# Optimization experiments

Measured on AMD Instinct MI355X. Metric: run time of the kernel, lower is better.

Reference implementation:

```python
import jax, jax.numpy as jnp
import numpy as np

SQRT_2PI = (2.0 * 3.14159) ** 0.5  # matches torch.jit.script gaussian constant


def setup_inputs() -> dict:
    key = jax.random.key(0)
    ks = jax.random.split(key, 7)
    B, N, R, K, H, HEADS = 4, 256, 4, 128, 512, 32
    rpe = jax.random.uniform(ks[0], (B, N, N, R), dtype=jnp.float32) * 5.0
    means = jax.random.uniform(ks[1], (R, K), dtype=jnp.float32, minval=0.0, maxval=3.0)
    stds = jax.random.uniform(ks[2], (R, K), dtype=jnp.float32, minval=0.0, maxval=3.0)
    W1 = jax.random.normal(ks[3], (H, R * K), dtype=jnp.float32) * (1.0 / (R * K) ** 0.5)
    b1 = jax.random.normal(ks[4], (H,), dtype=jnp.float32) * 0.01
    W2 = jax.random.normal(ks[5], (HEADS, H), dtype=jnp.float32) * (1.0 / H ** 0.5)
    b2 = jax.random.normal(ks[6], (HEADS,), dtype=jnp.float32) * 0.01
    return {"rpe": rpe, "means": means, "stds": stds, "W1": W1, "b1": b1, "W2": W2, "b2": b2}


def reference(rpe, means, stds, W1, b1, W2, b2):
    # GaussianLayer: (B,N,N,R) -> (B,N,N,R*K)
    std = jnp.abs(stds) + 0.01                      # (R,K)
    x = rpe[..., None]                              # (B,N,N,R,1)
    g = jnp.exp(-0.5 * ((x - means) / std) ** 2) / (SQRT_2PI * std)  # (B,N,N,R,K)
    B, N = rpe.shape[0], rpe.shape[1]
    g = g.reshape(B, N, N, -1)                      # (B,N,N,R*K)
    # NonLinear MLP: Linear -> gelu(exact) -> Linear
    h = jax.nn.gelu(jnp.einsum('bmnf,hf->bmnh', g, W1) + b1, approximate=False)
    out = jnp.einsum('bmnh,oh->bmno', h, W2) + b2   # (B,N,N,heads)
    # permute BATCH_HEAD_NODE_NODE = (0,3,1,2)
    return jnp.transpose(out, (0, 3, 1, 2))
```

## Files before the change

kernel.cpp:

```cpp
#include <hip/hip_runtime.h>
#include <hip/hip_bf16.h>

typedef __attribute__((ext_vector_type(8))) short bfrag8;
typedef __attribute__((ext_vector_type(4))) float f32x4;
typedef __attribute__((ext_vector_type(4))) unsigned int u32x4;

#define IS2_SCALE 0.84932180028801907f
#define W1_SCALE  0.46971724f

#if __has_builtin(__builtin_amdgcn_exp2f)
#define GEXP(x) __builtin_amdgcn_exp2f(x)
#else
__device__ __forceinline__ float gexp_asm(float x) {
  float r; asm("v_exp_f32 %0, %1" : "=v"(r) : "v"(x)); return r;
}
#define GEXP(x) gexp_asm(x)
#endif

__device__ __forceinline__ unsigned short f2bf(float x) {
  union { float f; unsigned u; } v; v.f = x;
  unsigned r = v.u + 0x7fffu + ((v.u >> 16) & 1u);
  return (unsigned short)(r >> 16);
}
__device__ __forceinline__ unsigned cvtpk(float lo, float hi) {
  unsigned r;
  asm("v_cvt_pk_bf16_f32 %0, %1, %2" : "=v"(r) : "v"(lo), "v"(hi));
  return r;
}
__device__ __forceinline__ float rcpa(float x) {
  float r; asm("v_rcp_f32 %0, %1" : "=v"(r) : "v"(x)); return r;
}
__device__ __forceinline__ float gelu_fast(float x) {
  float x2 = x * x;
  float w = __builtin_fmaf(x2, -0.1029488f, -2.3022078f);
  float e = GEXP(x * w);
  return x * rcpa(e + 1.0f);
}

__global__ void prep_kernel(const float* __restrict__ means, const float* __restrict__ stds,
                            const float* __restrict__ W1, const float* __restrict__ W2,
                            unsigned short* __restrict__ W1bf, unsigned short* __restrict__ W2bf,
                            float* __restrict__ prm ) {
  int t = blockIdx.x * blockDim.x + threadIdx.x;
  int stride = gridDim.x * blockDim.x;
  for (int i = t; i < 512 * 512; i += stride) W1bf[i] = f2bf(W1[i] * W1_SCALE);
  for (int i = t; i < 32 * 512; i += stride) W2bf[i] = f2bf(W2[i]);
  for (int i = t; i < 512; i += stride) {
    float s = fabsf(stds[i]) + 0.01f;
    float is2 = (1.0f / s) * IS2_SCALE;
    prm[2 * i] = -means[i] * is2;
    prm[2 * i + 1] = is2;
  }
}

__global__ __launch_bounds__(1024, 4) void fused_kernel(
    const float* __restrict__ rpe, const unsigned short* __restrict__ W1bf,
    const unsigned short* __restrict__ W2bf, const float* __restrict__ prm,
    const float* __restrict__ b1, const float* __restrict__ b2,
    float* __restrict__ out) {
  __shared__ __attribute__((aligned(16))) char lds[131072 + 4096 + 2048 + 2048];
  float* prm_s = (float*)(lds + 131072);
  float* rpe_s = (float*)(lds + 131072 + 4096);
  float* b1_s  = (float*)(lds + 131072 + 4096 + 2048);

  const int tid = threadIdx.x;
  const int rb = blockIdx.x * 128;

  if (tid < 512) rpe_s[tid] = rpe[rb * 4 + tid];
  prm_s[tid] = prm[tid];
  if (tid < 512) b1_s[tid] = b1[tid];

  int goff[2];
#pragma unroll
  for (int i = 0; i < 2; ++i) {
    int c = i * 1024 + tid;
    int j = ((c >> 6) << 4) + (c & 15);
    goff[i] = j * 512 + ((c >> 4) & 3) * 8;
  }
  const char* Wc = (const char*)W1bf;

#define STAGE(buf, kb)                                                          \
  {                                                                             \
    _Pragma("unroll") for (int i_ = 0; i_ < 2; ++i_) {                          \
      const void* gp = (const void*)(Wc + (size_t)goff[i_] * 2 + (kb) * 64);    \
      void* lp = (void*)(lds + (buf) * 32768 + i_ * 16384 + tid * 16);          \
      __builtin_amdgcn_global_load_lds(                                         \
          (const __attribute__((address_space(1))) void*)gp,                    \
          (__attribute__((address_space(3))) void*)lp, 16, 0, 0);               \
    }                                                                           \
  }

  STAGE(0, 0);
  __syncthreads();

  const int w = tid >> 6, l = tid & 63;
  const int lr = l & 15, lg = l >> 4;
  const int mw = w >> 2, nw = w & 3;
  const int r0 = mw * 32 + lr;

  const f32x4 xa = *(const f32x4*)&rpe_s[r0 * 4];
  const f32x4 xb = *(const f32x4*)&rpe_s[(r0 + 16) * 4];

  f32x4 zv = {0.f, 0.f, 0.f, 0.f};
  f32x4 acc[2][8];
#pragma unroll
  for (int mf = 0; mf < 2; ++mf)
#pragma unroll
    for (int nf = 0; nf < 8; ++nf) acc[mf][nf] = zv;

  const f32x4* prm4 = (const f32x4*)prm_s;
  int cur = 0;

#pragma unroll
  for (int kb = 0; kb < 16; ++kb) {
    if (kb < 15) STAGE(cur ^ 1, kb + 1);

    const int k0 = kb * 32 + lg * 8;
    const float x0 = xa[kb >> 2];
    const float x1 = xb[kb >> 2];
    unsigned pk0[4], pk1[4];
#pragma unroll
    for (int q = 0; q < 4; ++q) {
      f32x4 P = prm4[(k0 >> 1) + q];
      float u00 = __builtin_fmaf(x0, P[1], P[0]);
      float u01 = __builtin_fmaf(x0, P[3], P[2]);
      float u10 = __builtin_fmaf(x1, P[1], P[0]);
      float u11 = __builtin_fmaf(x1, P[3], P[2]);
      pk0[q] = cvtpk(P[1] * GEXP(-(u00 * u00)), P[3] * GEXP(-(u01 * u01)));
      pk1[q] = cvtpk(P[1] * GEXP(-(u10 * u10)), P[3] * GEXP(-(u11 * u11)));
    }
    u32x4 av0 = {pk0[0], pk0[1], pk0[2], pk0[3]};
    u32x4 av1 = {pk1[0], pk1[1], pk1[2], pk1[3]};
    bfrag8 a0 = __builtin_bit_cast(bfrag8, av0);
    bfrag8 a1 = __builtin_bit_cast(bfrag8, av1);

    if (kb < 15) {
      asm volatile("s_waitcnt vmcnt(2)" ::: "memory");
    } else {
      asm volatile("s_waitcnt vmcnt(0)" ::: "memory");
    }
    __builtin_amdgcn_s_barrier();
    __builtin_amdgcn_sched_barrier(0);

    const char* Bbase = lds + cur * 32768 + nw * 8192 + lg * 256 + lr * 16;
    __builtin_amdgcn_s_setprio(1);
#pragma unroll
    for (int nf = 0; nf < 8; ++nf) {
      bfrag8 b = *(const bfrag8*)(Bbase + nf * 1024);
      acc[0][nf] = __builtin_amdgcn_mfma_f32_16x16x32_bf16(a0, b, acc[0][nf], 0, 0, 0);
      acc[1][nf] = __builtin_amdgcn_mfma_f32_16x16x32_bf16(a1, b, acc[1][nf], 0, 0, 0);
    }
    __builtin_amdgcn_s_setprio(0);

    __builtin_amdgcn_s_barrier();
    cur ^= 1;
  }

  unsigned short* hbuf = (unsigned short*)lds;
#pragma unroll
  for (int mf = 0; mf < 2; ++mf) {
#pragma unroll
    for (int nf = 0; nf < 8; nf += 2) {
      int col0 = nw * 128 + nf * 16 + lr;
      int col1 = col0 + 16;
      float bb0 = b1_s[col0], bb1 = b1_s[col1];
#pragma unroll
      for (int bi = 0; bi < 4; ++bi) {
        float g0 = gelu_fast(acc[mf][nf][bi] + bb0);
        float g1 = gelu_fast(acc[mf][nf + 1][bi] + bb1);
        unsigned pr = cvtpk(g0, g1);
        int hrow = mw * 32 + mf * 16 + lg * 4 + bi;
        int base = hrow * 1024, sw = (hrow & 7) << 4;
        *(unsigned short*)((char*)hbuf + base + ((col0 * 2) ^ sw)) = (unsigned short)pr;
        *(unsigned short*)((char*)hbuf + base + ((col1 * 2) ^ sw)) = (unsigned short)(pr >> 16);
      }
    }
  }
  __syncthreads();

  const int rt = w >> 1, ct = w & 1;
  f32x4 acc2 = zv;
  const int row2 = rt * 16 + lr;
  for (int kb = 0; kb < 16; ++kb) {
    int cb = (kb * 64 + lg * 16) ^ ((row2 & 7) << 4);
    bfrag8 a = *(const bfrag8*)((char*)hbuf + row2 * 1024 + cb);
    bfrag8 b = *(const bfrag8*)(W2bf + (size_t)(ct * 16 + lr) * 512 + kb * 32 + lg * 8);
    acc2 = __builtin_amdgcn_mfma_f32_16x16x32_bf16(a, b, acc2, 0, 0, 0);
  }
  float b2v = b2[ct * 16 + lr];
  __syncthreads();

  float* ob = (float*)lds;
#pragma unroll
  for (int bi = 0; bi < 4; ++bi)
    ob[(rt * 16 + lg * 4 + bi) * 33 + (ct * 16 + lr)] = acc2[bi] + b2v;
  __syncthreads();

  const int bI = rb >> 16, mI = (rb >> 8) & 255, n0 = rb & 255;
  float* obase = out + ((size_t)(bI * 32) * 256 + mI) * 256 + n0;
#pragma unroll
  for (int p = 0; p < 4; ++p) {
    int e = tid + p * 1024;
    int o = e >> 7, i = e & 127;
    obase[(size_t)o * 65536 + i] = ob[i * 33 + o];
  }
#undef STAGE
}

extern "C" void kernel_launch(void* const* d_in, const int* in_sizes, int n_in,
                              void* d_out, int out_size, void* d_ws, size_t ws_size,
                              hipStream_t stream) {
  const float* rpe   = (const float*)d_in[0];
  const float* means = (const float*)d_in[1];
  const float* stds  = (const float*)d_in[2];
  const float* W1    = (const float*)d_in[3];
  const float* b1    = (const float*)d_in[4];
  const float* W2    = (const float*)d_in[5];
  const float* b2    = (const float*)d_in[6];
  float* out = (float*)d_out;

  char* ws = (char*)d_ws;
  unsigned short* W1bf = (unsigned short*)ws;
  unsigned short* W2bf = (unsigned short*)(ws + 524288);
  float* prm = (float*)(ws + 557056);

  prep_kernel<<<256, 256, 0, stream>>>(means, stds, W1, W2, W1bf, W2bf, prm);
  fused_kernel<<<2048, 1024, 0, stream>>>(rpe, W1bf, W2bf, prm, b1, b2, out);
}
```

Baseline: 276.0 us.

## Compute Gaussian A-fragments once per row group and share via LDS

Previously each of the four N-waves sharing the same rows recomputed the identical Gaussian basis fragments every k-step. Now only nw==0 waves compute them, one step ahead, and write them into a double-buffered 16KB LDS slot that the other waves read. This removes 3/4 of the exp/fma work but puts that work on a quarter of the waves, adds LDS traffic and a waitcnt, and raises LDS use per block, which may affect occupancy and balance. Note that gsl is indexed by lg*2048 + r0*16, and r0 only reaches 127 (2032 bytes), so the layout fits within the slot.

```diff
diff --git a/kernel.cpp b/kernel.cpp
--- a/kernel.cpp
+++ b/kernel.cpp
@@ -35,6 +35,27 @@
   float w = __builtin_fmaf(x2, -0.1029488f, -2.3022078f);
   float e = GEXP(x * w);
   return x * rcpa(e + 1.0f);
+}
+
+__device__ __forceinline__ void gauss_frags(const f32x4* prm4, const f32x4 xa, const f32x4 xb,
+                                            int kb, int lg, bfrag8* A0, bfrag8* A1) {
+  const int k0 = kb * 32 + lg * 8;
+  const float x0 = xa[kb >> 2], x1 = xb[kb >> 2];
+  unsigned pk0[4], pk1[4];
+#pragma unroll
+  for (int q = 0; q < 4; ++q) {
+    f32x4 P = prm4[(k0 >> 1) + q];
+    float u00 = __builtin_fmaf(x0, P[1], P[0]);
+    float u01 = __builtin_fmaf(x0, P[3], P[2]);
+    float u10 = __builtin_fmaf(x1, P[1], P[0]);
+    float u11 = __builtin_fmaf(x1, P[3], P[2]);
+    pk0[q] = cvtpk(P[1] * GEXP(-(u00 * u00)), P[3] * GEXP(-(u01 * u01)));
+    pk1[q] = cvtpk(P[1] * GEXP(-(u10 * u10)), P[3] * GEXP(-(u11 * u11)));
+  }
+  u32x4 av0 = {pk0[0], pk0[1], pk0[2], pk0[3]};
+  u32x4 av1 = {pk1[0], pk1[1], pk1[2], pk1[3]};
+  *A0 = __builtin_bit_cast(bfrag8, av0);
+  *A1 = __builtin_bit_cast(bfrag8, av1);
 }
 
 __global__ void prep_kernel(const float* __restrict__ means, const float* __restrict__ stds,
@@ -58,10 +79,11 @@
     const unsigned short* __restrict__ W2bf, const float* __restrict__ prm,
     const float* __restrict__ b1, const float* __restrict__ b2,
     float* __restrict__ out) {
-  __shared__ __attribute__((aligned(16))) char lds[131072 + 4096 + 2048 + 2048];
+  __shared__ __attribute__((aligned(16))) char lds[131072 + 4096 + 2048 + 2048 + 16384];
   float* prm_s = (float*)(lds + 131072);
   float* rpe_s = (float*)(lds + 131072 + 4096);
   float* b1_s  = (float*)(lds + 131072 + 4096 + 2048);
+  char*  gsl   = lds + 131072 + 4096 + 2048 + 2048;
 
   const int tid = threadIdx.x;
   const int rb = blockIdx.x * 128;
@@ -100,6 +122,18 @@
 
   const f32x4 xa = *(const f32x4*)&rpe_s[r0 * 4];
   const f32x4 xb = *(const f32x4*)&rpe_s[(r0 + 16) * 4];
+  const f32x4* prm4 = (const f32x4*)prm_s;
+
+  char* gw = gsl + lg * 2048 + r0 * 16;
+  const char* gr = gsl + lg * 2048 + r0 * 16;
+
+  bfrag8 acur0, acur1;
+  if (nw == 0) {
+    gauss_frags(prm4, xa, xb, 0, lg, &acur0, &acur1);
+    *(bfrag8*)(gw) = acur0;
+    *(bfrag8*)(gw + 256) = acur1;
+  }
+  __syncthreads();
 
   f32x4 zv = {0.f, 0.f, 0.f, 0.f};
   f32x4 acc[2][8];
@@ -108,31 +142,27 @@
 #pragma unroll
     for (int nf = 0; nf < 8; ++nf) acc[mf][nf] = zv;
 
-  const f32x4* prm4 = (const f32x4*)prm_s;
   int cur = 0;
 
 #pragma unroll
   for (int kb = 0; kb < 16; ++kb) {
     if (kb < 15) STAGE(cur ^ 1, kb + 1);
 
-    const int k0 = kb * 32 + lg * 8;
-    const float x0 = xa[kb >> 2];
-    const float x1 = xb[kb >> 2];
-    unsigned pk0[4], pk1[4];
-#pragma unroll
-    for (int q = 0; q < 4; ++q) {
-      f32x4 P = prm4[(k0 >> 1) + q];
-      float u00 = __builtin_fmaf(x0, P[1], P[0]);
-      float u01 = __builtin_fmaf(x0, P[3], P[2]);
-      float u10 = __builtin_fmaf(x1, P[1], P[0]);
-      float u11 = __builtin_fmaf(x1, P[3], P[2]);
-      pk0[q] = cvtpk(P[1] * GEXP(-(u00 * u00)), P[3] * GEXP(-(u01 * u01)));
-      pk1[q] = cvtpk(P[1] * GEXP(-(u10 * u10)), P[3] * GEXP(-(u11 * u11)));
-    }
-    u32x4 av0 = {pk0[0], pk0[1], pk0[2], pk0[3]};
-    u32x4 av1 = {pk1[0], pk1[1], pk1[2], pk1[3]};
-    bfrag8 a0 = __builtin_bit_cast(bfrag8, av0);
-    bfrag8 a1 = __builtin_bit_cast(bfrag8, av1);
+    const int slot = (kb & 1) * 8192;
+    bfrag8 a0, a1, an0, an1;
+    if (nw == 0) {
+      a0 = acur0; a1 = acur1;
+      if (kb < 15) {
+        gauss_frags(prm4, xa, xb, kb + 1, lg, &an0, &an1);
+        char* gwn = gw + (((kb + 1) & 1) * 8192);
+        *(bfrag8*)(gwn) = an0;
+        *(bfrag8*)(gwn + 256) = an1;
+        asm volatile("s_waitcnt lgkmcnt(0)" ::: "memory");
+      }
+    } else {
+      a0 = *(const bfrag8*)(gr + slot);
+      a1 = *(const bfrag8*)(gr + slot + 256);
+    }
 
     if (kb < 15) {
       asm volatile("s_waitcnt vmcnt(2)" ::: "memory");
@@ -153,6 +183,7 @@
     __builtin_amdgcn_s_setprio(0);
 
     __builtin_amdgcn_s_barrier();
+    if (nw == 0 && kb < 15) { acur0 = an0; acur1 = an1; }
     cur ^= 1;
   }
 
```

After: 281.7 us. 1.02x slower.

## Split hidden dimension across blocks with atomic accumulation of second GEMM

Applied to the files above, without the earlier changes.

Each block now processes 512 rows for one quarter of the hidden units, loading its entire W1 slice into LDS once instead of double-buffering K tiles. The second linear layer is computed per hidden-quarter and partial results are added into the output with fp32 atomics, after a new kernel initializes the output with b2. This removes per-tile barriers and the cross-wave hidden buffer, but quadruples Gaussian feature computation, adds an extra full output write pass and atomic traffic, and makes summation order nondeterministic.

```diff
diff --git a/kernel.cpp b/kernel.cpp
--- a/kernel.cpp
+++ b/kernel.cpp
@@ -35,6 +35,27 @@
   float w = __builtin_fmaf(x2, -0.1029488f, -2.3022078f);
   float e = GEXP(x * w);
   return x * rcpa(e + 1.0f);
+}
+
+__device__ __forceinline__ void gauss_frags(const f32x4* prm4, const f32x4 xa, const f32x4 xb,
+                                            int kb, int lg, bfrag8* A0, bfrag8* A1) {
+  const int k0 = kb * 32 + lg * 8;
+  const float x0 = xa[kb >> 2], x1 = xb[kb >> 2];
+  unsigned pk0[4], pk1[4];
+#pragma unroll
+  for (int q = 0; q < 4; ++q) {
+    f32x4 P = prm4[(k0 >> 1) + q];
+    float u00 = __builtin_fmaf(x0, P[1], P[0]);
+    float u01 = __builtin_fmaf(x0, P[3], P[2]);
+    float u10 = __builtin_fmaf(x1, P[1], P[0]);
+    float u11 = __builtin_fmaf(x1, P[3], P[2]);
+    pk0[q] = cvtpk(P[1] * GEXP(-(u00 * u00)), P[3] * GEXP(-(u01 * u01)));
+    pk1[q] = cvtpk(P[1] * GEXP(-(u10 * u10)), P[3] * GEXP(-(u11 * u11)));
+  }
+  u32x4 av0 = {pk0[0], pk0[1], pk0[2], pk0[3]};
+  u32x4 av1 = {pk1[0], pk1[1], pk1[2], pk1[3]};
+  *A0 = __builtin_bit_cast(bfrag8, av0);
+  *A1 = __builtin_bit_cast(bfrag8, av1);
 }
 
 __global__ void prep_kernel(const float* __restrict__ means, const float* __restrict__ stds,
@@ -53,158 +74,122 @@
   }
 }
 
+__global__ void init_out(const float* __restrict__ b2, float* __restrict__ out) {
+  int i = blockIdx.x * blockDim.x + threadIdx.x;
+  float v = b2[(i >> 14) & 31];
+  f32x4 vv = {v, v, v, v};
+  *reinterpret_cast<f32x4*>(out + (size_t)i * 4) = vv;
+}
+
 __global__ __launch_bounds__(1024, 4) void fused_kernel(
     const float* __restrict__ rpe, const unsigned short* __restrict__ W1bf,
     const unsigned short* __restrict__ W2bf, const float* __restrict__ prm,
-    const float* __restrict__ b1, const float* __restrict__ b2,
-    float* __restrict__ out) {
-  __shared__ __attribute__((aligned(16))) char lds[131072 + 4096 + 2048 + 2048];
+    const float* __restrict__ b1, float* __restrict__ out) {
+  __shared__ __attribute__((aligned(16))) char lds[131072 + 4096];
   float* prm_s = (float*)(lds + 131072);
-  float* rpe_s = (float*)(lds + 131072 + 4096);
-  float* b1_s  = (float*)(lds + 131072 + 4096 + 2048);
 
   const int tid = threadIdx.x;
-  const int rb = blockIdx.x * 128;
-
-  if (tid < 512) rpe_s[tid] = rpe[rb * 4 + tid];
+  const int bid = blockIdx.x;
+  const int c = bid & 3;
+  const int rb = (bid >> 2) * 512;
+
   prm_s[tid] = prm[tid];
-  if (tid < 512) b1_s[tid] = b1[tid];
-
-  int goff[2];
-#pragma unroll
-  for (int i = 0; i < 2; ++i) {
-    int c = i * 1024 + tid;
-    int j = ((c >> 6) << 4) + (c & 15);
-    goff[i] = j * 512 + ((c >> 4) & 3) * 8;
-  }
+
   const char* Wc = (const char*)W1bf;
-
-#define STAGE(buf, kb)                                                          \
-  {                                                                             \
-    _Pragma("unroll") for (int i_ = 0; i_ < 2; ++i_) {                          \
-      const void* gp = (const void*)(Wc + (size_t)goff[i_] * 2 + (kb) * 64);    \
-      void* lp = (void*)(lds + (buf) * 32768 + i_ * 16384 + tid * 16);          \
-      __builtin_amdgcn_global_load_lds(                                         \
-          (const __attribute__((address_space(1))) void*)gp,                    \
-          (__attribute__((address_space(3))) void*)lp, 16, 0, 0);               \
-    }                                                                           \
-  }
-
-  STAGE(0, 0);
+#pragma unroll
+  for (int i = 0; i < 8; ++i) {
+    int c16 = i * 1024 + tid;
+    int ks = c16 >> 9;
+    int J  = (c16 >> 6) & 7;
+    int lgs = (c16 >> 4) & 3;
+    int jr = c16 & 15;
+    const void* gp = Wc + ((size_t)(c * 128 + J * 16 + jr) * 512 + ks * 32 + lgs * 8) * 2;
+    void* lp = lds + c16 * 16;
+    __builtin_amdgcn_global_load_lds(
+        (const __attribute__((address_space(1))) void*)gp,
+        (__attribute__((address_space(3))) void*)lp, 16, 0, 0);
+  }
   __syncthreads();
 
   const int w = tid >> 6, l = tid & 63;
   const int lr = l & 15, lg = l >> 4;
-  const int mw = w >> 2, nw = w & 3;
-  const int r0 = mw * 32 + lr;
-
-  const f32x4 xa = *(const f32x4*)&rpe_s[r0 * 4];
-  const f32x4 xb = *(const f32x4*)&rpe_s[(r0 + 16) * 4];
+  const int r0w = rb + w * 32;
+
+  const f32x4 xa = *(const f32x4*)(rpe + (size_t)(r0w + lr) * 4);
+  const f32x4 xb = *(const f32x4*)(rpe + (size_t)(r0w + 16 + lr) * 4);
+  const f32x4* prm4 = (const f32x4*)prm_s;
 
   f32x4 zv = {0.f, 0.f, 0.f, 0.f};
   f32x4 acc[2][8];
 #pragma unroll
   for (int mf = 0; mf < 2; ++mf)
 #pragma unroll
-    for (int nf = 0; nf < 8; ++nf) acc[mf][nf] = zv;
-
-  const f32x4* prm4 = (const f32x4*)prm_s;
-  int cur = 0;
-
-#pragma unroll
-  for (int kb = 0; kb < 16; ++kb) {
-    if (kb < 15) STAGE(cur ^ 1, kb + 1);
-
-    const int k0 = kb * 32 + lg * 8;
-    const float x0 = xa[kb >> 2];
-    const float x1 = xb[kb >> 2];
-    unsigned pk0[4], pk1[4];
-#pragma unroll
-    for (int q = 0; q < 4; ++q) {
-      f32x4 P = prm4[(k0 >> 1) + q];
-      float u00 = __builtin_fmaf(x0, P[1], P[0]);
-      float u01 = __builtin_fmaf(x0, P[3], P[2]);
-      float u10 = __builtin_fmaf(x1, P[1], P[0]);
-      float u11 = __builtin_fmaf(x1, P[3], P[2]);
-      pk0[q] = cvtpk(P[1] * GEXP(-(u00 * u00)), P[3] * GEXP(-(u01 * u01)));
-      pk1[q] = cvtpk(P[1] * GEXP(-(u10 * u10)), P[3] * GEXP(-(u11 * u11)));
+    for (int J = 0; J < 8; ++J) acc[mf][J] = zv;
+
+#pragma unroll
+  for (int ks = 0; ks < 16; ++ks) {
+    bfrag8 a0, a1;
+    gauss_frags(prm4, xa, xb, ks, lg, &a0, &a1);
+    const char* Bb = lds + ks * 8192 + lg * 256 + lr * 16;
+#pragma unroll
+    for (int J = 0; J < 8; ++J) {
+      bfrag8 b = *(const bfrag8*)(Bb + J * 1024);
+      acc[0][J] = __builtin_amdgcn_mfma_f32_16x16x32_bf16(a0, b, acc[0][J], 0, 0, 0);
+      acc[1][J] = __builtin_amdgcn_mfma_f32_16x16x32_bf16(a1, b, acc[1][J], 0, 0, 0);
     }
-    u32x4 av0 = {pk0[0], pk0[1], pk0[2], pk0[3]};
-    u32x4 av1 = {pk1[0], pk1[1], pk1[2], pk1[3]};
-    bfrag8 a0 = __builtin_bit_cast(bfrag8, av0);
-    bfrag8 a1 = __builtin_bit_cast(bfrag8, av1);
-
-    if (kb < 15) {
-      asm volatile("s_waitcnt vmcnt(2)" ::: "memory");
-    } else {
-      asm volatile("s_waitcnt vmcnt(0)" ::: "memory");
-    }
-    __builtin_amdgcn_s_barrier();
-    __builtin_amdgcn_sched_barrier(0);
-
-    const char* Bbase = lds + cur * 32768 + nw * 8192 + lg * 256 + lr * 16;
-    __builtin_amdgcn_s_setprio(1);
-#pragma unroll
-    for (int nf = 0; nf < 8; ++nf) {
-      bfrag8 b = *(const bfrag8*)(Bbase + nf * 1024);
-      acc[0][nf] = __builtin_amdgcn_mfma_f32_16x16x32_bf16(a0, b, acc[0][nf], 0, 0, 0);
-      acc[1][nf] = __builtin_amdgcn_mfma_f32_16x16x32_bf16(a1, b, acc[1][nf], 0, 0, 0);
-    }
-    __builtin_amdgcn_s_setprio(0);
-
-    __builtin_amdgcn_s_barrier();
-    cur ^= 1;
-  }
-
-  unsigned short* hbuf = (unsigned short*)lds;
+  }
+  __syncthreads();
+
+  char* scr = lds + w * 8192;
 #pragma unroll
   for (int mf = 0; mf < 2; ++mf) {
 #pragma unroll
-    for (int nf = 0; nf < 8; nf += 2) {
-      int col0 = nw * 128 + nf * 16 + lr;
-      int col1 = col0 + 16;
-      float bb0 = b1_s[col0], bb1 = b1_s[col1];
-#pragma unroll
-      for (int bi = 0; bi < 4; ++bi) {
-        float g0 = gelu_fast(acc[mf][nf][bi] + bb0);
-        float g1 = gelu_fast(acc[mf][nf + 1][bi] + bb1);
-        unsigned pr = cvtpk(g0, g1);
-        int hrow = mw * 32 + mf * 16 + lg * 4 + bi;
-        int base = hrow * 1024, sw = (hrow & 7) << 4;
-        *(unsigned short*)((char*)hbuf + base + ((col0 * 2) ^ sw)) = (unsigned short)pr;
-        *(unsigned short*)((char*)hbuf + base + ((col1 * 2) ^ sw)) = (unsigned short)(pr >> 16);
+    for (int J = 0; J < 8; ++J) {
+      float bb = b1[c * 128 + J * 16 + lr];
+#pragma unroll
+      for (int q = 0; q < 4; ++q) {
+        float g = gelu_fast(acc[mf][J][q] + bb);
+        int r = mf * 16 + lg * 4 + q;
+        int byte = (r * 256 + (J * 16 + lr) * 2) ^ ((r & 7) << 4);
+        *(unsigned short*)(scr + byte) = f2bf(g);
       }
     }
   }
-  __syncthreads();
-
-  const int rt = w >> 1, ct = w & 1;
-  f32x4 acc2 = zv;
-  const int row2 = rt * 16 + lr;
-  for (int kb = 0; kb < 16; ++kb) {
-    int cb = (kb * 64 + lg * 16) ^ ((row2 & 7) << 4);
-    bfrag8 a = *(const bfrag8*)((char*)hbuf + row2 * 1024 + cb);
-    bfrag8 b = *(const bfrag8*)(W2bf + (size_t)(ct * 16 + lr) * 512 + kb * 32 + lg * 8);
-    acc2 = __builtin_amdgcn_mfma_f32_16x16x32_bf16(a, b, acc2, 0, 0, 0);
-  }
-  float b2v = b2[ct * 16 + lr];
-  __syncthreads();
-
-  float* ob = (float*)lds;
-#pragma unroll
-  for (int bi = 0; bi < 4; ++bi)
-    ob[(rt * 16 + lg * 4 + bi) * 33 + (ct * 16 + lr)] = acc2[bi] + b2v;
-  __syncthreads();
-
-  const int bI = rb >> 16, mI = (rb >> 8) & 255, n0 = rb & 255;
-  float* obase = out + ((size_t)(bI * 32) * 256 + mI) * 256 + n0;
-#pragma unroll
-  for (int p = 0; p < 4; ++p) {
-    int e = tid + p * 1024;
-    int o = e >> 7, i = e & 127;
-    obase[(size_t)o * 65536 + i] = ob[i * 33 + o];
-  }
-#undef STAGE
+
+  bfrag8 w2f[2][4];
+#pragma unroll
+  for (int og = 0; og < 2; ++og)
+#pragma unroll
+    for (int kk = 0; kk < 4; ++kk)
+      w2f[og][kk] = *(const bfrag8*)(W2bf + (size_t)(og * 16 + lr) * 512 + c * 128 + kk * 32 + lg * 8);
+
+  asm volatile("s_waitcnt lgkmcnt(0)" ::: "memory");
+  f32x4 acc2[2][2];
+  acc2[0][0] = zv; acc2[0][1] = zv; acc2[1][0] = zv; acc2[1][1] = zv;
+#pragma unroll
+  for (int rf = 0; rf < 2; ++rf) {
+#pragma unroll
+    for (int kk = 0; kk < 4; ++kk) {
+      int r = rf * 16 + lr;
+      int byte = (r * 256 + kk * 64 + lg * 16) ^ ((r & 7) << 4);
+      bfrag8 a = *(const bfrag8*)(scr + byte);
+      acc2[rf][0] = __builtin_amdgcn_mfma_f32_16x16x32_bf16(a, w2f[0][kk], acc2[rf][0], 0, 0, 0);
+      acc2[rf][1] = __builtin_amdgcn_mfma_f32_16x16x32_bf16(a, w2f[1][kk], acc2[rf][1], 0, 0, 0);
+    }
+  }
+
+  const int bI = rb >> 16;
+  float* ob = out + (size_t)bI * 2097152 + (rb & 65535) + w * 32;
+#pragma unroll
+  for (int rf = 0; rf < 2; ++rf)
+#pragma unroll
+    for (int og = 0; og < 2; ++og)
+#pragma unroll
+      for (int q = 0; q < 4; ++q) {
+        int o = og * 16 + lr;
+        int r = rf * 16 + lg * 4 + q;
+        atomicAdd(ob + (size_t)o * 65536 + r, acc2[rf][og][q]);
+      }
 }
 
 extern "C" void kernel_launch(void* const* d_in, const int* in_sizes, int n_in,
@@ -225,5 +210,6 @@
   float* prm = (float*)(ws + 557056);
 
   prep_kernel<<<256, 256, 0, stream>>>(means, stds, W1, W2, W1bf, W2bf, prm);
-  fused_kernel<<<2048, 1024, 0, stream>>>(rpe, W1bf, W2bf, prm, b1, b2, out);
-}
+  init_out<<<8192, 256, 0, stream>>>(b2, out);
+  fused_kernel<<<2048, 1024, 0, stream>>>(rpe, W1bf, W2bf, prm, b1, out);
+}
```

New measurement: 505.3 us. +83.0%, slower.

## Triple-buffer W1 LDS tiles and software-pipeline B fragments and Gaussian features

Applied to the files above, without the earlier changes.

The first GEMM's K-loop moves from double to triple buffering of W1 tiles in LDS, prefetching two stages ahead with a single barrier per iteration instead of two. B fragments are split into two register halves so the next stage's first half is read from LDS while the second half's MFMAs run. The Gaussian A-fragments for the next K-block are computed after the current MFMAs to overlap VALU exp work with matrix work. The cost is higher register pressure from the extra fragment buffers and a full vmcnt(0) wait each iteration.

```diff
diff --git a/kernel.cpp b/kernel.cpp
--- a/kernel.cpp
+++ b/kernel.cpp
@@ -35,6 +35,27 @@
   float w = __builtin_fmaf(x2, -0.1029488f, -2.3022078f);
   float e = GEXP(x * w);
   return x * rcpa(e + 1.0f);
+}
+
+__device__ __forceinline__ void gauss_frags(const f32x4* prm4, const f32x4 xa, const f32x4 xb,
+                                            int kb, int lg, bfrag8* A0, bfrag8* A1) {
+  const int k0 = kb * 32 + lg * 8;
+  const float x0 = xa[kb >> 2], x1 = xb[kb >> 2];
+  unsigned pk0[4], pk1[4];
+#pragma unroll
+  for (int q = 0; q < 4; ++q) {
+    f32x4 P = prm4[(k0 >> 1) + q];
+    float u00 = __builtin_fmaf(x0, P[1], P[0]);
+    float u01 = __builtin_fmaf(x0, P[3], P[2]);
+    float u10 = __builtin_fmaf(x1, P[1], P[0]);
+    float u11 = __builtin_fmaf(x1, P[3], P[2]);
+    pk0[q] = cvtpk(P[1] * GEXP(-(u00 * u00)), P[3] * GEXP(-(u01 * u01)));
+    pk1[q] = cvtpk(P[1] * GEXP(-(u10 * u10)), P[3] * GEXP(-(u11 * u11)));
+  }
+  u32x4 av0 = {pk0[0], pk0[1], pk0[2], pk0[3]};
+  u32x4 av1 = {pk1[0], pk1[1], pk1[2], pk1[3]};
+  *A0 = __builtin_bit_cast(bfrag8, av0);
+  *A1 = __builtin_bit_cast(bfrag8, av1);
 }
 
 __global__ void prep_kernel(const float* __restrict__ means, const float* __restrict__ stds,
@@ -91,6 +112,7 @@
   }
 
   STAGE(0, 0);
+  STAGE(1, 1);
   __syncthreads();
 
   const int w = tid >> 6, l = tid & 63;
@@ -100,6 +122,7 @@
 
   const f32x4 xa = *(const f32x4*)&rpe_s[r0 * 4];
   const f32x4 xb = *(const f32x4*)&rpe_s[(r0 + 16) * 4];
+  const f32x4* prm4 = (const f32x4*)prm_s;
 
   f32x4 zv = {0.f, 0.f, 0.f, 0.f};
   f32x4 acc[2][8];
@@ -108,53 +131,50 @@
 #pragma unroll
     for (int nf = 0; nf < 8; ++nf) acc[mf][nf] = zv;
 
-  const f32x4* prm4 = (const f32x4*)prm_s;
-  int cur = 0;
+  bfrag8 fA[4], fB[4];
+  {
+    const char* Bb = lds + nw * 8192 + lg * 256 + lr * 16;
+#pragma unroll
+    for (int nf = 0; nf < 4; ++nf) fA[nf] = *(const bfrag8*)(Bb + nf * 1024);
+  }
+  bfrag8 a0, a1;
+  gauss_frags(prm4, xa, xb, 0, lg, &a0, &a1);
 
 #pragma unroll
   for (int kb = 0; kb < 16; ++kb) {
-    if (kb < 15) STAGE(cur ^ 1, kb + 1);
-
-    const int k0 = kb * 32 + lg * 8;
-    const float x0 = xa[kb >> 2];
-    const float x1 = xb[kb >> 2];
-    unsigned pk0[4], pk1[4];
-#pragma unroll
-    for (int q = 0; q < 4; ++q) {
-      f32x4 P = prm4[(k0 >> 1) + q];
-      float u00 = __builtin_fmaf(x0, P[1], P[0]);
-      float u01 = __builtin_fmaf(x0, P[3], P[2]);
-      float u10 = __builtin_fmaf(x1, P[1], P[0]);
-      float u11 = __builtin_fmaf(x1, P[3], P[2]);
-      pk0[q] = cvtpk(P[1] * GEXP(-(u00 * u00)), P[3] * GEXP(-(u01 * u01)));
-      pk1[q] = cvtpk(P[1] * GEXP(-(u10 * u10)), P[3] * GEXP(-(u11 * u11)));
-    }
-    u32x4 av0 = {pk0[0], pk0[1], pk0[2], pk0[3]};
-    u32x4 av1 = {pk1[0], pk1[1], pk1[2], pk1[3]};
-    bfrag8 a0 = __builtin_bit_cast(bfrag8, av0);
-    bfrag8 a1 = __builtin_bit_cast(bfrag8, av1);
-
-    if (kb < 15) {
-      asm volatile("s_waitcnt vmcnt(2)" ::: "memory");
-    } else {
-      asm volatile("s_waitcnt vmcnt(0)" ::: "memory");
-    }
+    asm volatile("s_waitcnt vmcnt(0)" ::: "memory");
     __builtin_amdgcn_s_barrier();
     __builtin_amdgcn_sched_barrier(0);
-
-    const char* Bbase = lds + cur * 32768 + nw * 8192 + lg * 256 + lr * 16;
+    if (kb < 14) STAGE((kb + 2) % 3, kb + 2);
+
+    const char* Bb = lds + (kb % 3) * 32768 + nw * 8192 + lg * 256 + lr * 16;
     __builtin_amdgcn_s_setprio(1);
 #pragma unroll
-    for (int nf = 0; nf < 8; ++nf) {
-      bfrag8 b = *(const bfrag8*)(Bbase + nf * 1024);
-      acc[0][nf] = __builtin_amdgcn_mfma_f32_16x16x32_bf16(a0, b, acc[0][nf], 0, 0, 0);
-      acc[1][nf] = __builtin_amdgcn_mfma_f32_16x16x32_bf16(a1, b, acc[1][nf], 0, 0, 0);
+    for (int nf = 0; nf < 4; ++nf) fB[nf] = *(const bfrag8*)(Bb + (nf + 4) * 1024);
+#pragma unroll
+    for (int nf = 0; nf < 4; ++nf) {
+      acc[0][nf] = __builtin_amdgcn_mfma_f32_16x16x32_bf16(a0, fA[nf], acc[0][nf], 0, 0, 0);
+      acc[1][nf] = __builtin_amdgcn_mfma_f32_16x16x32_bf16(a1, fA[nf], acc[1][nf], 0, 0, 0);
     }
     __builtin_amdgcn_s_setprio(0);
-
-    __builtin_amdgcn_s_barrier();
-    cur ^= 1;
-  }
+    __builtin_amdgcn_sched_barrier(0);
+
+    __builtin_amdgcn_s_setprio(1);
+    if (kb < 15) {
+      const char* Bn = lds + ((kb + 1) % 3) * 32768 + nw * 8192 + lg * 256 + lr * 16;
+#pragma unroll
+      for (int nf = 0; nf < 4; ++nf) fA[nf] = *(const bfrag8*)(Bn + nf * 1024);
+    }
+#pragma unroll
+    for (int nf = 0; nf < 4; ++nf) {
+      acc[0][nf + 4] = __builtin_amdgcn_mfma_f32_16x16x32_bf16(a0, fB[nf], acc[0][nf + 4], 0, 0, 0);
+      acc[1][nf + 4] = __builtin_amdgcn_mfma_f32_16x16x32_bf16(a1, fB[nf], acc[1][nf + 4], 0, 0, 0);
+    }
+    __builtin_amdgcn_s_setprio(0);
+    if (kb < 15) gauss_frags(prm4, xa, xb, kb + 1, lg, &a0, &a1);
+    __builtin_amdgcn_sched_barrier(0);
+  }
+  __syncthreads();
 
   unsigned short* hbuf = (unsigned short*)lds;
 #pragma unroll
```

New measurement: 271.8 us. About the same (-1.5%).
